# Kernel tuning notes

Measured on AMD Instinct MI355X. Metric: run time of the kernel, lower is better.

## Reference

```python
import jax, jax.numpy as jnp
import numpy as np

N, IN_DIM, HID, E = 2048, 128, 64, 32768
EPS = 1e-5  # torch BatchNorm1d / LayerNorm default eps


def setup_inputs() -> dict:
    key = jax.random.key(0)
    ks = jax.random.split(key, 12)
    s = 0.05
    return {
        "h": jax.random.normal(ks[0], (N, IN_DIM), jnp.float32),
        "local": jax.random.normal(ks[1], (N, IN_DIM), jnp.float32),
        "e": jax.random.normal(ks[2], (E, HID), jnp.float32),
        "src": jax.random.randint(ks[3], (E,), 0, N, jnp.int32),
        "dst": jax.random.randint(ks[4], (E,), 0, N, jnp.int32),
        "ln_w": jnp.ones((IN_DIM,), jnp.float32),
        "ln_b": jnp.zeros((IN_DIM,), jnp.float32),
        "conv_w": jax.random.normal(ks[5], (1, 2, 3), jnp.float32) * 0.3,
        "conv_b": jnp.zeros((1,), jnp.float32),
        "W1": jax.random.normal(ks[6], (IN_DIM, HID * HID), jnp.float32) * s,
        "b1": jnp.zeros((HID * HID,), jnp.float32),
        "Wp2": jax.random.normal(ks[7], (IN_DIM, HID), jnp.float32) * s,
        "bp2": jnp.zeros((HID,), jnp.float32),
        "W2": jax.random.normal(ks[8], (IN_DIM, HID), jnp.float32) * s,
        "b2": jnp.zeros((HID,), jnp.float32),
        "W3": jax.random.normal(ks[9], (HID, HID), jnp.float32) * s,
        "b3": jnp.zeros((HID,), jnp.float32),
        "bng_g": jnp.ones((HID,), jnp.float32),
        "bng_b": jnp.zeros((HID,), jnp.float32),
        "bnG_g": jnp.ones((HID,), jnp.float32),
        "bnG_b": jnp.zeros((HID,), jnp.float32),
        "bnL_g": jnp.ones((HID,), jnp.float32),
        "bnL_b": jnp.zeros((HID,), jnp.float32),
    }


def _bn_eval(x, g, b):
    # BatchNorm1d in eval mode, running_mean=0, running_var=1
    return x * (g / jnp.sqrt(1.0 + EPS)) + b


def _layernorm(x, w, b):
    mu = jnp.mean(x, axis=-1, keepdims=True)
    var = jnp.var(x, axis=-1, keepdims=True)
    return (x - mu) / jnp.sqrt(var + EPS) * w + b


def reference(h, local, e, src, dst, ln_w, ln_b, conv_w, conv_b,
              W1, b1, Wp2, bp2, W2, b2, W3, b3,
              bng_g, bng_b, bnG_g, bnG_b, bnL_g, bnL_b):
    # ---- local edge branch ----
    edge = jnp.stack([local[src], local[dst]], axis=1)  # [E, 2, in_dim]
    edge = _layernorm(edge, ln_w, ln_b)
    # Conv1d(2 -> 1, k=3, pad=1) over the in_dim axis
    lr_local = jax.lax.conv_general_dilated(
        edge, conv_w, window_strides=(1,), padding=[(1, 1)],
        dimension_numbers=("NCH", "OIH", "NCH"))[:, 0, :] + conv_b  # [E, in_dim]
    lr_local = jax.nn.relu(lr_local)  # dropout is identity in eval
    lr_local = lr_local @ W2 + b2  # [E, hid]

    # ---- global edge branch ----
    p1 = jax.nn.relu(h @ W1 + b1).reshape(h.shape[0], HID, HID)  # [N, hid(d), hid(k)]
    p2 = jax.nn.relu(h @ Wp2 + bp2)  # [N, hid(k)]
    # mm[i, j, d] = sum_k p1[i, d, k] * p2[j, k]; gather only needed edges
    lr_global = jnp.einsum("edk,ek->ed", p1[src], p2[dst])  # [E, hid]
    lr_global = _bn_eval(lr_global, bng_g, bng_b) @ W3 + b3
    lr_global = jax.nn.relu(_bn_eval(lr_global, bnG_g, bnG_b))

    lr_local = jax.nn.relu(_bn_eval(lr_local, bnL_g, bnL_b))
    return lr_local + lr_global + e
```

## Files before the change

kernel.cpp:

```cpp
#include <hip/hip_runtime.h>

#define N_NODES 2048
#define IN_DIM 128
#define HID 64
#define N_EDGES 32768
#define EPS 1e-5f

typedef short short8 __attribute__((ext_vector_type(8)));
typedef float f32x4 __attribute__((ext_vector_type(4)));

__device__ __forceinline__ float relu_f(float x) { return fmaxf(x, 0.f); }

__device__ __forceinline__ unsigned short f2bf(float f) {
  unsigned int u = __float_as_uint(f);
  u = (u + 0x7fffu + ((u >> 16) & 1u)) >> 16;
  return (unsigned short)u;
}
__device__ __forceinline__ float bf2f(unsigned short h) {
  return __uint_as_float(((unsigned int)h) << 16);
}
__device__ __forceinline__ short8 pack8(const float* f) {
  short8 o;
  #pragma unroll
  for (int i = 0; i < 8; ++i) o[i] = (short)f2bf(f[i]);
  return o;
}

__global__ __launch_bounds__(256) void ln_kernel(
    const float* __restrict__ local, const float* __restrict__ ln_w,
    const float* __restrict__ ln_b, float* __restrict__ out)
{
  int wave = threadIdx.x >> 6;
  int lane = threadIdx.x & 63;
  int row = blockIdx.x * 4 + wave;
  const float* x = local + (size_t)row * IN_DIM;
  float x0 = x[lane], x1 = x[lane + 64];
  float s1 = x0 + x1;
  float s2 = x0 * x0 + x1 * x1;
  #pragma unroll
  for (int off = 32; off > 0; off >>= 1) {
    s1 += __shfl_xor(s1, off);
    s2 += __shfl_xor(s2, off);
  }
  float mean = s1 * (1.f / IN_DIM);
  float var = s2 * (1.f / IN_DIM) - mean * mean;
  float rstd = rsqrtf(var + EPS);
  float* o = out + (size_t)row * IN_DIM;
  o[lane]      = (x0 - mean) * rstd * ln_w[lane] + ln_b[lane];
  o[lane + 64] = (x1 - mean) * rstd * ln_w[lane + 64] + ln_b[lane + 64];
}

__global__ __launch_bounds__(256) void p2_kernel(
    const float* __restrict__ h, const float* __restrict__ Wp2,
    const float* __restrict__ bp2, unsigned short* __restrict__ p2b)
{
  __shared__ float hs[4][IN_DIM];
  int wv = threadIdx.x >> 6, l = threadIdx.x & 63;
  int i = blockIdx.x * 4 + wv;
  hs[wv][l] = h[(size_t)i * IN_DIM + l];
  hs[wv][l + 64] = h[(size_t)i * IN_DIM + 64 + l];
  float acc = bp2[l];
  #pragma unroll 8
  for (int m = 0; m < IN_DIM; ++m) acc += hs[wv][m] * Wp2[m * HID + l];
  p2b[(size_t)i * HID + l] = f2bf(relu_f(acc));
}

__global__ __launch_bounds__(256) void prep_misc(
    const float* __restrict__ h, const float* __restrict__ W2,
    const float* __restrict__ W3, unsigned short* __restrict__ hb,
    unsigned short* __restrict__ w2tb, unsigned short* __restrict__ w3tb)
{
  int b = blockIdx.x, t = threadIdx.x;
  if (b < 256) {
    int idx = (b * 256 + t) * 4;
    float4 v = *(const float4*)(h + idx);
    ushort4 o;
    o.x = f2bf(v.x); o.y = f2bf(v.y); o.z = f2bf(v.z); o.w = f2bf(v.w);
    *(ushort4*)(hb + idx) = o;
  } else if (b == 256) {
    for (int i = t; i < IN_DIM * HID; i += 256) {
      int x = i >> 6, j = i & 63;
      w2tb[j * IN_DIM + x] = f2bf(W2[i]);
    }
  } else {
    for (int i = t; i < HID * HID; i += 256) {
      int k = i >> 6, j = i & 63;
      w3tb[j * HID + k] = f2bf(W3[i]);
    }
  }
}

__global__ __launch_bounds__(256) void tr_w1(
    const float* __restrict__ W1, unsigned short* __restrict__ w1t)
{
  __shared__ float tile[32][33];
  int n0 = blockIdx.x * 32, k0 = blockIdx.y * 32;
  int tx = threadIdx.x & 31, ty = threadIdx.x >> 5;
  #pragma unroll
  for (int r = 0; r < 4; ++r)
    tile[ty + 8 * r][tx] = W1[(size_t)(k0 + ty + 8 * r) * 4096 + n0 + tx];
  __syncthreads();
  #pragma unroll
  for (int r = 0; r < 4; ++r)
    w1t[(size_t)(n0 + ty + 8 * r) * 128 + k0 + tx] = f2bf(tile[tx][ty + 8 * r]);
}

__global__ __launch_bounds__(256) void p1_gemm(
    const unsigned short* __restrict__ hb,
    const unsigned short* __restrict__ w1t,
    const float* __restrict__ b1,
    unsigned short* __restrict__ p1b)
{
  int t = threadIdx.x;
  int w = t >> 6, l = t & 63;
  int lr = l & 15, lq = l >> 4;
  int bm = (blockIdx.x & 15) * 128;
  int bn = (blockIdx.x >> 4) * 128;
  int m0 = bm + w * 32;

  f32x4 acc[2][8];
  #pragma unroll
  for (int mi = 0; mi < 2; ++mi)
    #pragma unroll
    for (int ni = 0; ni < 8; ++ni) acc[mi][ni] = (f32x4){0.f, 0.f, 0.f, 0.f};

  #pragma unroll
  for (int k0 = 0; k0 < 128; k0 += 32) {
    short8 a[2], b[8];
    #pragma unroll
    for (int mi = 0; mi < 2; ++mi)
      a[mi] = *(const short8*)(hb + (size_t)(m0 + mi * 16 + lr) * 128 + k0 + lq * 8);
    #pragma unroll
    for (int ni = 0; ni < 8; ++ni)
      b[ni] = *(const short8*)(w1t + (size_t)(bn + ni * 16 + lr) * 128 + k0 + lq * 8);
    #pragma unroll
    for (int mi = 0; mi < 2; ++mi)
      #pragma unroll
      for (int ni = 0; ni < 8; ++ni)
        acc[mi][ni] = __builtin_amdgcn_mfma_f32_16x16x32_bf16(a[mi], b[ni], acc[mi][ni], 0, 0, 0);
  }

  #pragma unroll
  for (int mi = 0; mi < 2; ++mi)
    #pragma unroll
    for (int ni = 0; ni < 8; ++ni) {
      int col = bn + ni * 16 + lr;
      float bias = b1[col];
      #pragma unroll
      for (int r = 0; r < 4; ++r) {
        int row = m0 + mi * 16 + lq * 4 + r;
        p1b[(size_t)row * 4096 + col] = f2bf(relu_f(acc[mi][ni][r] + bias));
      }
    }
}

__global__ void hist_kernel(const int* __restrict__ src, int* __restrict__ cnt) {
  int e = blockIdx.x * 256 + threadIdx.x;
  atomicAdd(&cnt[src[e]], 1);
}

__global__ __launch_bounds__(256) void scan_kernel(
    const int* __restrict__ cnt, int* __restrict__ start,
    int* __restrict__ cursor, int* __restrict__ ptile)
{
  __shared__ int part[256];
  __shared__ int part2[256];
  int t = threadIdx.x;
  int loc[8], locT[8];
  int s = 0, s2 = 0;
  #pragma unroll
  for (int i = 0; i < 8; ++i) {
    int c = cnt[t * 8 + i];
    loc[i] = s;  s += c;
    locT[i] = s2; s2 += (c + 15) >> 4;
  }
  part[t] = s; part2[t] = s2;
  __syncthreads();
  for (int off = 1; off < 256; off <<= 1) {
    int v = (t >= off) ? part[t - off] : 0;
    int v2 = (t >= off) ? part2[t - off] : 0;
    __syncthreads();
    part[t] += v; part2[t] += v2;
    __syncthreads();
  }
  int base = (t == 0) ? 0 : part[t - 1];
  int base2 = (t == 0) ? 0 : part2[t - 1];
  #pragma unroll
  for (int i = 0; i < 8; ++i) {
    int v = base + loc[i];
    start[t * 8 + i] = v;
    cursor[t * 8 + i] = v;
    ptile[t * 8 + i] = base2 + locT[i];
  }
  if (t == 255) { start[N_NODES] = part[255]; ptile[N_NODES] = part2[255]; }
}

__global__ void scatter_kernel(const int* __restrict__ src,
                               int* __restrict__ cursor, int* __restrict__ perm) {
  int e = blockIdx.x * 256 + threadIdx.x;
  int p = atomicAdd(&cursor[src[e]], 1);
  perm[p] = e;
}

__global__ void build_tiles(const int* __restrict__ cnt, const int* __restrict__ start,
                            const int* __restrict__ ptile, const int* __restrict__ perm,
                            int* __restrict__ tile_src, int* __restrict__ perm_padded) {
  int i = blockIdx.x * 256 + threadIdx.x;
  int deg = cnt[i], s0 = start[i], t0 = ptile[i];
  int nt = (deg + 15) >> 4;
  for (int k = 0; k < nt; ++k) {
    int tid = t0 + k;
    tile_src[tid] = i;
    for (int j = 0; j < 16; ++j) {
      int pos = k * 16 + j;
      perm_padded[tid * 16 + j] = (pos < deg) ? perm[s0 + pos] : -1;
    }
  }
}

__global__ __launch_bounds__(256) void gather_mfma(
    const unsigned short* __restrict__ p1b, const unsigned short* __restrict__ p2b,
    const int* __restrict__ dst, const int* __restrict__ perm_padded,
    const int* __restrict__ tile_src, const int* __restrict__ ptile,
    const unsigned short* __restrict__ w3tb, const float* __restrict__ b3,
    const float* __restrict__ bng_g, const float* __restrict__ bng_b,
    const float* __restrict__ bnG_g, const float* __restrict__ bnG_b,
    float* __restrict__ gbuf)
{
  __shared__ float gs[4][16][68];
  const int t = threadIdx.x;
  const int w = t >> 6, l = t & 63;
  const int lr = l & 15, lq = l >> 4;
  const int n_tiles = ptile[N_NODES];
  const float rs = rsqrtf(1.f + EPS);

  float bngG[4], bngB[4], bnGG[4], bnGB[4], b3c[4];
  #pragma unroll
  for (int ni = 0; ni < 4; ++ni) {
    int col = ni * 16 + lr;
    bngG[ni] = bng_g[col] * rs; bngB[ni] = bng_b[col];
    bnGG[ni] = bnG_g[col] * rs; bnGB[ni] = bnG_b[col];
    b3c[ni] = b3[col];
  }

  for (int tile = blockIdx.x * 4 + w; tile < n_tiles; tile += gridDim.x * 4) {
    const int srcn = tile_src[tile];
    const int eidx = perm_padded[tile * 16 + lr];
    const int dn = (eidx >= 0) ? dst[eidx] : 0;

    const unsigned short* p2r = p2b + (size_t)dn * HID + lq * 8;
    short8 a0 = *(const short8*)(p2r);
    short8 a1 = *(const short8*)(p2r + 32);

    const unsigned short* pr = p1b + (size_t)srcn * 4096 + lr * 64 + lq * 8;
    f32x4 c[4];
    #pragma unroll
    for (int ni = 0; ni < 4; ++ni) {
      c[ni] = (f32x4){0.f, 0.f, 0.f, 0.f};
      short8 b0 = *(const short8*)(pr + ni * 1024);
      short8 b1 = *(const short8*)(pr + ni * 1024 + 32);
      c[ni] = __builtin_amdgcn_mfma_f32_16x16x32_bf16(a0, b0, c[ni], 0, 0, 0);
      c[ni] = __builtin_amdgcn_mfma_f32_16x16x32_bf16(a1, b1, c[ni], 0, 0, 0);
    }

    #pragma unroll
    for (int ni = 0; ni < 4; ++ni)
      #pragma unroll
      for (int r = 0; r < 4; ++r)
        gs[w][lq * 4 + r][ni * 16 + lr] = c[ni][r] * bngG[ni] + bngB[ni];
    asm volatile("s_waitcnt lgkmcnt(0)" ::: "memory");

    short8 ga0 = pack8(&gs[w][lr][lq * 8]);
    short8 ga1 = pack8(&gs[w][lr][32 + lq * 8]);

    const unsigned short* wr = w3tb + lr * HID + lq * 8;
    f32x4 u[4];
    #pragma unroll
    for (int ni = 0; ni < 4; ++ni) {
      u[ni] = (f32x4){0.f, 0.f, 0.f, 0.f};
      short8 b0 = *(const short8*)(wr + ni * 1024);
      short8 b1 = *(const short8*)(wr + ni * 1024 + 32);
      u[ni] = __builtin_amdgcn_mfma_f32_16x16x32_bf16(ga0, b0, u[ni], 0, 0, 0);
      u[ni] = __builtin_amdgcn_mfma_f32_16x16x32_bf16(ga1, b1, u[ni], 0, 0, 0);
    }

    int er[4];
    #pragma unroll
    for (int r = 0; r < 4; ++r) er[r] = perm_padded[tile * 16 + lq * 4 + r];
    #pragma unroll
    for (int ni = 0; ni < 4; ++ni) {
      int col = ni * 16 + lr;
      #pragma unroll
      for (int r = 0; r < 4; ++r)
        if (er[r] >= 0)
          gbuf[(size_t)er[r] * HID + col] =
              relu_f((u[ni][r] + b3c[ni]) * bnGG[ni] + bnGB[ni]);
    }
  }
}

__global__ __launch_bounds__(256) void final_kernel(
    const float* __restrict__ lnl, const int* __restrict__ src,
    const int* __restrict__ dst, const float* __restrict__ conv_w,
    const float* __restrict__ conv_b, const unsigned short* __restrict__ w2tb,
    const float* __restrict__ b2,
    const float* __restrict__ bnL_g, const float* __restrict__ bnL_b,
    const float* __restrict__ gbuf, const float* __restrict__ e_in,
    float* __restrict__ out)
{
  __shared__ float lns[32][132];
  __shared__ unsigned short rc[16][136];
  __shared__ int nodebuf[32];

  const int eb = blockIdx.x * 16;
  const int t = threadIdx.x;
  const int w = t >> 6, l = t & 63;
  const int lr = l & 15, lq = l >> 4;
  const float rs = rsqrtf(1.f + EPS);

  if (t < 32) nodebuf[t] = (t & 1) ? dst[eb + (t >> 1)] : src[eb + (t >> 1)];
  __syncthreads();
  #pragma unroll
  for (int r = 0; r < 4; ++r) {
    int flat = (r * 256 + t) * 4;
    int rr = flat >> 7, x = flat & 127;
    *(float4*)&lns[rr][x] = *(const float4*)(lnl + (size_t)nodebuf[rr] * IN_DIM + x);
  }
  __syncthreads();
  {
    float cw0 = conv_w[0], cw1 = conv_w[1], cw2 = conv_w[2];
    float cw3 = conv_w[3], cw4 = conv_w[4], cw5 = conv_w[5];
    float cb = conv_b[0];
    #pragma unroll
    for (int r = 0; r < 8; ++r) {
      int flat = r * 256 + t;
      int ei = flat >> 7, x = flat & 127;
      const float* a = &lns[2 * ei][0];
      const float* b = &lns[2 * ei + 1][0];
      float am = (x > 0) ? a[x - 1] : 0.f;
      float ap = (x < 127) ? a[x + 1] : 0.f;
      float bm = (x > 0) ? b[x - 1] : 0.f;
      float bp = (x < 127) ? b[x + 1] : 0.f;
      rc[ei][x] = f2bf(relu_f(cw0 * am + cw1 * a[x] + cw2 * ap +
                              cw3 * bm + cw4 * b[x] + cw5 * bp + cb));
    }
  }
  __syncthreads();
  f32x4 u = (f32x4){0.f, 0.f, 0.f, 0.f};
  #pragma unroll
  for (int ks = 0; ks < 4; ++ks) {
    short8 a = *(const short8*)&rc[lr][ks * 32 + lq * 8];
    short8 b = *(const short8*)(w2tb + (size_t)(w * 16 + lr) * IN_DIM + ks * 32 + lq * 8);
    u = __builtin_amdgcn_mfma_f32_16x16x32_bf16(a, b, u, 0, 0, 0);
  }
  int col = w * 16 + lr;
  float g = bnL_g[col] * rs, bb = bnL_b[col], b2c = b2[col];
  #pragma unroll
  for (int r = 0; r < 4; ++r) {
    int e = eb + lq * 4 + r;
    float vl = relu_f((u[r] + b2c) * g + bb);
    out[(size_t)e * HID + col] = vl + gbuf[(size_t)e * HID + col] + e_in[(size_t)e * HID + col];
  }
}

extern "C" void kernel_launch(void* const* d_in, const int* in_sizes, int n_in,
                              void* d_out, int out_size, void* d_ws, size_t ws_size,
                              hipStream_t stream) {
  const float* h      = (const float*)d_in[0];
  const float* local  = (const float*)d_in[1];
  const float* e_in   = (const float*)d_in[2];
  const int*   src    = (const int*)d_in[3];
  const int*   dst    = (const int*)d_in[4];
  const float* ln_w   = (const float*)d_in[5];
  const float* ln_b   = (const float*)d_in[6];
  const float* conv_w = (const float*)d_in[7];
  const float* conv_b = (const float*)d_in[8];
  const float* W1     = (const float*)d_in[9];
  const float* b1     = (const float*)d_in[10];
  const float* Wp2    = (const float*)d_in[11];
  const float* bp2    = (const float*)d_in[12];
  const float* W2     = (const float*)d_in[13];
  const float* b2     = (const float*)d_in[14];
  const float* W3     = (const float*)d_in[15];
  const float* b3     = (const float*)d_in[16];
  const float* bng_g  = (const float*)d_in[17];
  const float* bng_b  = (const float*)d_in[18];
  const float* bnG_g  = (const float*)d_in[19];
  const float* bnG_b  = (const float*)d_in[20];
  const float* bnL_g  = (const float*)d_in[21];
  const float* bnL_b  = (const float*)d_in[22];
  float* out = (float*)d_out;

  char* p = (char*)d_ws;
  unsigned short* p1b = (unsigned short*)p; p += (size_t)N_NODES * HID * HID * 2;
  unsigned short* p2b = (unsigned short*)p; p += (size_t)N_NODES * HID * 2;
  float* lnl  = (float*)p; p += (size_t)N_NODES * IN_DIM * 4;
  float* gbuf = (float*)p; p += (size_t)N_EDGES * HID * 4;
  unsigned short* hb   = (unsigned short*)p; p += (size_t)N_NODES * IN_DIM * 2;
  unsigned short* w1t  = (unsigned short*)p; p += (size_t)4096 * 128 * 2;
  unsigned short* w2tb = (unsigned short*)p; p += (size_t)HID * IN_DIM * 2;
  unsigned short* w3tb = (unsigned short*)p; p += (size_t)HID * HID * 2;
  int* cnt    = (int*)p; p += N_NODES * 4;
  int* cursor = (int*)p; p += N_NODES * 4;
  int* startb = (int*)p; p += (N_NODES + 1) * 4;
  int* ptile  = (int*)p; p += (N_NODES + 1) * 4;
  int* perm   = (int*)p; p += (size_t)N_EDGES * 4;
  int* tile_src    = (int*)p; p += 4096 * 4;
  int* perm_padded = (int*)p; p += (size_t)4096 * 16 * 4;

  hipMemsetAsync(cnt, 0, N_NODES * sizeof(int), stream);

  prep_misc<<<258, 256, 0, stream>>>(h, W2, W3, hb, w2tb, w3tb);
  tr_w1<<<dim3(128, 4), 256, 0, stream>>>(W1, w1t);
  ln_kernel<<<N_NODES / 4, 256, 0, stream>>>(local, ln_w, ln_b, lnl);
  p2_kernel<<<N_NODES / 4, 256, 0, stream>>>(h, Wp2, bp2, p2b);
  p1_gemm<<<512, 256, 0, stream>>>(hb, w1t, b1, p1b);
  hist_kernel<<<N_EDGES / 256, 256, 0, stream>>>(src, cnt);
  scan_kernel<<<1, 256, 0, stream>>>(cnt, startb, cursor, ptile);
  scatter_kernel<<<N_EDGES / 256, 256, 0, stream>>>(src, cursor, perm);
  build_tiles<<<N_NODES / 256, 256, 0, stream>>>(cnt, startb, ptile, perm, tile_src, perm_padded);
  gather_mfma<<<512, 256, 0, stream>>>(p1b, p2b, dst, perm_padded, tile_src, ptile,
                                       w3tb, b3, bng_g, bng_b, bnG_g, bnG_b, gbuf);
  final_kernel<<<N_EDGES / 16, 256, 0, stream>>>(lnl, src, dst, conv_w, conv_b,
                                                 w2tb, b2, bnL_g, bnL_b, gbuf, e_in, out);
}
```

Measured before the change: 188.0 us.

## Fuse local branch into edge MFMA kernel and merge prep kernels

Merges the separate prep kernels (bf16 casts, W1 transpose, layernorm, p2) into one launch. The local conv+W2 branch moves into the per-tile global edge kernel, so the fp32 gbuf round-trip and the final kernel disappear. Layernorm output is stored in bf16. The CSR build drops the perm/build_tiles pass and scatters straight into padded tiles. p1_gemm is retiled with swapped operands to allow vectorized bf16 stores. The cost is extra LDS traffic and a heavier edge kernel, plus a 0xFF memset of perm_padded.

```diff
diff --git a/kernel.cpp b/kernel.cpp
--- a/kernel.cpp
+++ b/kernel.cpp
@@ -5,6 +5,7 @@
 #define HID 64
 #define N_EDGES 32768
 #define EPS 1e-5f
+#define MAX_TILES 4608
 
 typedef short short8 __attribute__((ext_vector_type(8)));
 typedef float f32x4 __attribute__((ext_vector_type(4)));
@@ -26,83 +27,73 @@
   return o;
 }
 
-__global__ __launch_bounds__(256) void ln_kernel(
+__global__ __launch_bounds__(256) void prep_all(
+    const float* __restrict__ h, const float* __restrict__ W2,
+    const float* __restrict__ W3, const float* __restrict__ W1,
     const float* __restrict__ local, const float* __restrict__ ln_w,
-    const float* __restrict__ ln_b, float* __restrict__ out)
+    const float* __restrict__ ln_b, const float* __restrict__ Wp2,
+    const float* __restrict__ bp2,
+    unsigned short* __restrict__ hb, unsigned short* __restrict__ w2tb,
+    unsigned short* __restrict__ w3tb, unsigned short* __restrict__ w1t,
+    unsigned short* __restrict__ lnlb, unsigned short* __restrict__ p2b)
 {
-  int wave = threadIdx.x >> 6;
-  int lane = threadIdx.x & 63;
-  int row = blockIdx.x * 4 + wave;
-  const float* x = local + (size_t)row * IN_DIM;
-  float x0 = x[lane], x1 = x[lane + 64];
-  float s1 = x0 + x1;
-  float s2 = x0 * x0 + x1 * x1;
-  #pragma unroll
-  for (int off = 32; off > 0; off >>= 1) {
-    s1 += __shfl_xor(s1, off);
-    s2 += __shfl_xor(s2, off);
-  }
-  float mean = s1 * (1.f / IN_DIM);
-  float var = s2 * (1.f / IN_DIM) - mean * mean;
-  float rstd = rsqrtf(var + EPS);
-  float* o = out + (size_t)row * IN_DIM;
-  o[lane]      = (x0 - mean) * rstd * ln_w[lane] + ln_b[lane];
-  o[lane + 64] = (x1 - mean) * rstd * ln_w[lane + 64] + ln_b[lane + 64];
-}
-
-__global__ __launch_bounds__(256) void p2_kernel(
-    const float* __restrict__ h, const float* __restrict__ Wp2,
-    const float* __restrict__ bp2, unsigned short* __restrict__ p2b)
-{
+  __shared__ float tile[32][33];
   __shared__ float hs[4][IN_DIM];
-  int wv = threadIdx.x >> 6, l = threadIdx.x & 63;
-  int i = blockIdx.x * 4 + wv;
-  hs[wv][l] = h[(size_t)i * IN_DIM + l];
-  hs[wv][l + 64] = h[(size_t)i * IN_DIM + 64 + l];
-  float acc = bp2[l];
-  #pragma unroll 8
-  for (int m = 0; m < IN_DIM; ++m) acc += hs[wv][m] * Wp2[m * HID + l];
-  p2b[(size_t)i * HID + l] = f2bf(relu_f(acc));
-}
-
-__global__ __launch_bounds__(256) void prep_misc(
-    const float* __restrict__ h, const float* __restrict__ W2,
-    const float* __restrict__ W3, unsigned short* __restrict__ hb,
-    unsigned short* __restrict__ w2tb, unsigned short* __restrict__ w3tb)
-{
-  int b = blockIdx.x, t = threadIdx.x;
+  const int b = blockIdx.x, t = threadIdx.x;
+
   if (b < 256) {
     int idx = (b * 256 + t) * 4;
     float4 v = *(const float4*)(h + idx);
-    ushort4 o;
-    o.x = f2bf(v.x); o.y = f2bf(v.y); o.z = f2bf(v.z); o.w = f2bf(v.w);
+    ushort4 o; o.x = f2bf(v.x); o.y = f2bf(v.y); o.z = f2bf(v.z); o.w = f2bf(v.w);
     *(ushort4*)(hb + idx) = o;
   } else if (b == 256) {
     for (int i = t; i < IN_DIM * HID; i += 256) {
       int x = i >> 6, j = i & 63;
       w2tb[j * IN_DIM + x] = f2bf(W2[i]);
     }
-  } else {
+  } else if (b == 257) {
     for (int i = t; i < HID * HID; i += 256) {
       int k = i >> 6, j = i & 63;
       w3tb[j * HID + k] = f2bf(W3[i]);
     }
-  }
-}
-
-__global__ __launch_bounds__(256) void tr_w1(
-    const float* __restrict__ W1, unsigned short* __restrict__ w1t)
-{
-  __shared__ float tile[32][33];
-  int n0 = blockIdx.x * 32, k0 = blockIdx.y * 32;
-  int tx = threadIdx.x & 31, ty = threadIdx.x >> 5;
-  #pragma unroll
-  for (int r = 0; r < 4; ++r)
-    tile[ty + 8 * r][tx] = W1[(size_t)(k0 + ty + 8 * r) * 4096 + n0 + tx];
-  __syncthreads();
-  #pragma unroll
-  for (int r = 0; r < 4; ++r)
-    w1t[(size_t)(n0 + ty + 8 * r) * 128 + k0 + tx] = f2bf(tile[tx][ty + 8 * r]);
+  } else if (b < 258 + 512) {
+    int b2 = b - 258;
+    int n0 = (b2 & 127) * 32, k0 = (b2 >> 7) * 32;
+    int tx = t & 31, ty = t >> 5;
+    #pragma unroll
+    for (int r = 0; r < 4; ++r)
+      tile[ty + 8 * r][tx] = W1[(size_t)(k0 + ty + 8 * r) * 4096 + n0 + tx];
+    __syncthreads();
+    #pragma unroll
+    for (int r = 0; r < 4; ++r)
+      w1t[(size_t)(n0 + ty + 8 * r) * 128 + k0 + tx] = f2bf(tile[tx][ty + 8 * r]);
+  } else if (b < 770 + 512) {
+    int wave = t >> 6, lane = t & 63;
+    int row = (b - 770) * 4 + wave;
+    const float* x = local + (size_t)row * IN_DIM;
+    float x0 = x[lane], x1 = x[lane + 64];
+    float s1 = x0 + x1, s2 = x0 * x0 + x1 * x1;
+    #pragma unroll
+    for (int off = 32; off > 0; off >>= 1) {
+      s1 += __shfl_xor(s1, off);
+      s2 += __shfl_xor(s2, off);
+    }
+    float mean = s1 * (1.f / IN_DIM);
+    float var = s2 * (1.f / IN_DIM) - mean * mean;
+    float rstd = rsqrtf(var + EPS);
+    unsigned short* o = lnlb + (size_t)row * IN_DIM;
+    o[lane]      = f2bf((x0 - mean) * rstd * ln_w[lane] + ln_b[lane]);
+    o[lane + 64] = f2bf((x1 - mean) * rstd * ln_w[lane + 64] + ln_b[lane + 64]);
+  } else {
+    int wv = t >> 6, l = t & 63;
+    int i = (b - 1282) * 4 + wv;
+    hs[wv][l] = h[(size_t)i * IN_DIM + l];
+    hs[wv][l + 64] = h[(size_t)i * IN_DIM + 64 + l];
+    float acc = bp2[l];
+    #pragma unroll 8
+    for (int m = 0; m < IN_DIM; ++m) acc += hs[wv][m] * Wp2[m * HID + l];
+    p2b[(size_t)i * HID + l] = f2bf(relu_f(acc));
+  }
 }
 
 __global__ __launch_bounds__(256) void p1_gemm(
@@ -111,47 +102,38 @@
     const float* __restrict__ b1,
     unsigned short* __restrict__ p1b)
 {
-  int t = threadIdx.x;
-  int w = t >> 6, l = t & 63;
-  int lr = l & 15, lq = l >> 4;
-  int bm = (blockIdx.x & 15) * 128;
-  int bn = (blockIdx.x >> 4) * 128;
-  int m0 = bm + w * 32;
-
-  f32x4 acc[2][8];
-  #pragma unroll
-  for (int mi = 0; mi < 2; ++mi)
-    #pragma unroll
-    for (int ni = 0; ni < 8; ++ni) acc[mi][ni] = (f32x4){0.f, 0.f, 0.f, 0.f};
+  const int t = threadIdx.x;
+  const int w = t >> 6, l = t & 63;
+  const int lr = l & 15, lq = l >> 4;
+  const int bm = (blockIdx.x & 31) * 64;
+  const int bn = (blockIdx.x >> 5) * 128;
+  const int m0 = bm + w * 16;
+
+  f32x4 acc[8];
+  #pragma unroll
+  for (int ni = 0; ni < 8; ++ni) acc[ni] = (f32x4){0.f, 0.f, 0.f, 0.f};
 
   #pragma unroll
   for (int k0 = 0; k0 < 128; k0 += 32) {
-    short8 a[2], b[8];
-    #pragma unroll
-    for (int mi = 0; mi < 2; ++mi)
-      a[mi] = *(const short8*)(hb + (size_t)(m0 + mi * 16 + lr) * 128 + k0 + lq * 8);
-    #pragma unroll
-    for (int ni = 0; ni < 8; ++ni)
-      b[ni] = *(const short8*)(w1t + (size_t)(bn + ni * 16 + lr) * 128 + k0 + lq * 8);
-    #pragma unroll
-    for (int mi = 0; mi < 2; ++mi)
-      #pragma unroll
-      for (int ni = 0; ni < 8; ++ni)
-        acc[mi][ni] = __builtin_amdgcn_mfma_f32_16x16x32_bf16(a[mi], b[ni], acc[mi][ni], 0, 0, 0);
-  }
-
-  #pragma unroll
-  for (int mi = 0; mi < 2; ++mi)
+    short8 bmf = *(const short8*)(hb + (size_t)(m0 + lr) * 128 + k0 + lq * 8);
     #pragma unroll
     for (int ni = 0; ni < 8; ++ni) {
-      int col = bn + ni * 16 + lr;
-      float bias = b1[col];
-      #pragma unroll
-      for (int r = 0; r < 4; ++r) {
-        int row = m0 + mi * 16 + lq * 4 + r;
-        p1b[(size_t)row * 4096 + col] = f2bf(relu_f(acc[mi][ni][r] + bias));
-      }
-    }
+      short8 a = *(const short8*)(w1t + (size_t)(bn + ni * 16 + lr) * 128 + k0 + lq * 8);
+      acc[ni] = __builtin_amdgcn_mfma_f32_16x16x32_bf16(a, bmf, acc[ni], 0, 0, 0);
+    }
+  }
+  const int m = m0 + lr;
+  #pragma unroll
+  for (int ni = 0; ni < 8; ++ni) {
+    int n = bn + ni * 16 + lq * 4;
+    float4 bv = *(const float4*)&b1[n];
+    ushort4 o;
+    o.x = f2bf(relu_f(acc[ni][0] + bv.x));
+    o.y = f2bf(relu_f(acc[ni][1] + bv.y));
+    o.z = f2bf(relu_f(acc[ni][2] + bv.z));
+    o.w = f2bf(relu_f(acc[ni][3] + bv.w));
+    *(ushort4*)&p1b[(size_t)m * 4096 + n] = o;
+  }
 }
 
 __global__ void hist_kernel(const int* __restrict__ src, int* __restrict__ cnt) {
@@ -160,107 +142,107 @@
 }
 
 __global__ __launch_bounds__(256) void scan_kernel(
-    const int* __restrict__ cnt, int* __restrict__ start,
-    int* __restrict__ cursor, int* __restrict__ ptile)
+    const int* __restrict__ cnt, int* __restrict__ ptile, int* __restrict__ tile_src)
 {
-  __shared__ int part[256];
   __shared__ int part2[256];
   int t = threadIdx.x;
-  int loc[8], locT[8];
-  int s = 0, s2 = 0;
+  int locT[8];
+  int s2 = 0;
   #pragma unroll
   for (int i = 0; i < 8; ++i) {
-    int c = cnt[t * 8 + i];
-    loc[i] = s;  s += c;
-    locT[i] = s2; s2 += (c + 15) >> 4;
-  }
-  part[t] = s; part2[t] = s2;
+    locT[i] = s2;
+    s2 += (cnt[t * 8 + i] + 15) >> 4;
+  }
+  part2[t] = s2;
   __syncthreads();
   for (int off = 1; off < 256; off <<= 1) {
-    int v = (t >= off) ? part[t - off] : 0;
-    int v2 = (t >= off) ? part2[t - off] : 0;
+    int v = (t >= off) ? part2[t - off] : 0;
     __syncthreads();
-    part[t] += v; part2[t] += v2;
+    part2[t] += v;
     __syncthreads();
   }
-  int base = (t == 0) ? 0 : part[t - 1];
   int base2 = (t == 0) ? 0 : part2[t - 1];
   #pragma unroll
   for (int i = 0; i < 8; ++i) {
-    int v = base + loc[i];
-    start[t * 8 + i] = v;
-    cursor[t * 8 + i] = v;
-    ptile[t * 8 + i] = base2 + locT[i];
-  }
-  if (t == 255) { start[N_NODES] = part[255]; ptile[N_NODES] = part2[255]; }
-}
-
-__global__ void scatter_kernel(const int* __restrict__ src,
-                               int* __restrict__ cursor, int* __restrict__ perm) {
+    int node = t * 8 + i;
+    int tb = base2 + locT[i];
+    ptile[node] = tb;
+    int nt = (cnt[node] + 15) >> 4;
+    for (int k = 0; k < nt; ++k) tile_src[tb + k] = node;
+  }
+  if (t == 255) ptile[N_NODES] = part2[255];
+}
+
+__global__ void scatter_kernel(const int* __restrict__ src, const int* __restrict__ ptile,
+                               int* __restrict__ cursor, int* __restrict__ perm_padded) {
   int e = blockIdx.x * 256 + threadIdx.x;
-  int p = atomicAdd(&cursor[src[e]], 1);
-  perm[p] = e;
-}
-
-__global__ void build_tiles(const int* __restrict__ cnt, const int* __restrict__ start,
-                            const int* __restrict__ ptile, const int* __restrict__ perm,
-                            int* __restrict__ tile_src, int* __restrict__ perm_padded) {
-  int i = blockIdx.x * 256 + threadIdx.x;
-  int deg = cnt[i], s0 = start[i], t0 = ptile[i];
-  int nt = (deg + 15) >> 4;
-  for (int k = 0; k < nt; ++k) {
-    int tid = t0 + k;
-    tile_src[tid] = i;
-    for (int j = 0; j < 16; ++j) {
-      int pos = k * 16 + j;
-      perm_padded[tid * 16 + j] = (pos < deg) ? perm[s0 + pos] : -1;
-    }
-  }
-}
-
-__global__ __launch_bounds__(256) void gather_mfma(
+  int s = src[e];
+  int r = atomicAdd(&cursor[s], 1);
+  perm_padded[ptile[s] * 16 + r] = e;
+}
+
+__global__ __launch_bounds__(256) void edge_mfma(
     const unsigned short* __restrict__ p1b, const unsigned short* __restrict__ p2b,
+    const unsigned short* __restrict__ lnlb,
     const int* __restrict__ dst, const int* __restrict__ perm_padded,
     const int* __restrict__ tile_src, const int* __restrict__ ptile,
-    const unsigned short* __restrict__ w3tb, const float* __restrict__ b3,
+    const unsigned short* __restrict__ w2tb, const unsigned short* __restrict__ w3tb,
+    const float* __restrict__ conv_w, const float* __restrict__ conv_b,
+    const float* __restrict__ b2, const float* __restrict__ b3,
     const float* __restrict__ bng_g, const float* __restrict__ bng_b,
     const float* __restrict__ bnG_g, const float* __restrict__ bnG_b,
-    float* __restrict__ gbuf)
+    const float* __restrict__ bnL_g, const float* __restrict__ bnL_b,
+    const float* __restrict__ e_in, float* __restrict__ out)
 {
   __shared__ float gs[4][16][68];
+  __shared__ unsigned short ln1s[4][16][136];
+  __shared__ unsigned short ln0s[4][136];
+
   const int t = threadIdx.x;
   const int w = t >> 6, l = t & 63;
   const int lr = l & 15, lq = l >> 4;
   const int n_tiles = ptile[N_NODES];
   const float rs = rsqrtf(1.f + EPS);
 
-  float bngG[4], bngB[4], bnGG[4], bnGB[4], b3c[4];
+  float bngG[4], bngB[4], bnGG[4], bnGB[4], b3c[4], bnLG[4], bnLB[4], b2c[4];
   #pragma unroll
   for (int ni = 0; ni < 4; ++ni) {
     int col = ni * 16 + lr;
     bngG[ni] = bng_g[col] * rs; bngB[ni] = bng_b[col];
     bnGG[ni] = bnG_g[col] * rs; bnGB[ni] = bnG_b[col];
-    b3c[ni] = b3[col];
-  }
+    bnLG[ni] = bnL_g[col] * rs; bnLB[ni] = bnL_b[col];
+    b3c[ni] = b3[col]; b2c[ni] = b2[col];
+  }
+  const float cw0 = conv_w[0], cw1 = conv_w[1], cw2 = conv_w[2];
+  const float cw3 = conv_w[3], cw4 = conv_w[4], cw5 = conv_w[5];
+  const float cb = conv_b[0];
 
   for (int tile = blockIdx.x * 4 + w; tile < n_tiles; tile += gridDim.x * 4) {
     const int srcn = tile_src[tile];
     const int eidx = perm_padded[tile * 16 + lr];
     const int dn = (eidx >= 0) ? dst[eidx] : 0;
 
+    {
+      const unsigned short* r1 = lnlb + (size_t)dn * IN_DIM + lq * 32;
+      #pragma unroll
+      for (int c2 = 0; c2 < 4; ++c2)
+        *(uint4*)&ln1s[w][lr][lq * 32 + c2 * 8] = *(const uint4*)(r1 + c2 * 8);
+      if (l < 32)
+        *(ushort4*)&ln0s[w][l * 4] = *(const ushort4*)(lnlb + (size_t)srcn * IN_DIM + l * 4);
+    }
+
     const unsigned short* p2r = p2b + (size_t)dn * HID + lq * 8;
     short8 a0 = *(const short8*)(p2r);
     short8 a1 = *(const short8*)(p2r + 32);
-
     const unsigned short* pr = p1b + (size_t)srcn * 4096 + lr * 64 + lq * 8;
     f32x4 c[4];
     #pragma unroll
     for (int ni = 0; ni < 4; ++ni) {
       c[ni] = (f32x4){0.f, 0.f, 0.f, 0.f};
-      short8 b0 = *(const short8*)(pr + ni * 1024);
-      short8 b1 = *(const short8*)(pr + ni * 1024 + 32);
-      c[ni] = __builtin_amdgcn_mfma_f32_16x16x32_bf16(a0, b0, c[ni], 0, 0, 0);
-      c[ni] = __builtin_amdgcn_mfma_f32_16x16x32_bf16(a1, b1, c[ni], 0, 0, 0);
+      short8 pb0 = *(const short8*)(pr + ni * 1024);
+      short8 pb1 = *(const short8*)(pr + ni * 1024 + 32);
+      c[ni] = __builtin_amdgcn_mfma_f32_16x16x32_bf16(a0, pb0, c[ni], 0, 0, 0);
+      c[ni] = __builtin_amdgcn_mfma_f32_16x16x32_bf16(a1, pb1, c[ni], 0, 0, 0);
     }
 
     #pragma unroll
@@ -269,97 +251,63 @@
       for (int r = 0; r < 4; ++r)
         gs[w][lq * 4 + r][ni * 16 + lr] = c[ni][r] * bngG[ni] + bngB[ni];
     asm volatile("s_waitcnt lgkmcnt(0)" ::: "memory");
-
     short8 ga0 = pack8(&gs[w][lr][lq * 8]);
     short8 ga1 = pack8(&gs[w][lr][32 + lq * 8]);
 
-    const unsigned short* wr = w3tb + lr * HID + lq * 8;
+    const unsigned short* wr3 = w3tb + lr * HID + lq * 8;
     f32x4 u[4];
     #pragma unroll
     for (int ni = 0; ni < 4; ++ni) {
       u[ni] = (f32x4){0.f, 0.f, 0.f, 0.f};
-      short8 b0 = *(const short8*)(wr + ni * 1024);
-      short8 b1 = *(const short8*)(wr + ni * 1024 + 32);
-      u[ni] = __builtin_amdgcn_mfma_f32_16x16x32_bf16(ga0, b0, u[ni], 0, 0, 0);
-      u[ni] = __builtin_amdgcn_mfma_f32_16x16x32_bf16(ga1, b1, u[ni], 0, 0, 0);
+      short8 wb0 = *(const short8*)(wr3 + ni * 1024);
+      short8 wb1 = *(const short8*)(wr3 + ni * 1024 + 32);
+      u[ni] = __builtin_amdgcn_mfma_f32_16x16x32_bf16(ga0, wb0, u[ni], 0, 0, 0);
+      u[ni] = __builtin_amdgcn_mfma_f32_16x16x32_bf16(ga1, wb1, u[ni], 0, 0, 0);
+    }
+
+    asm volatile("s_waitcnt vmcnt(0) lgkmcnt(0)" ::: "memory");
+    f32x4 v[4];
+    #pragma unroll
+    for (int ni = 0; ni < 4; ++ni) v[ni] = (f32x4){0.f, 0.f, 0.f, 0.f};
+    #pragma unroll
+    for (int ks = 0; ks < 4; ++ks) {
+      short8 af;
+      #pragma unroll
+      for (int j = 0; j < 8; ++j) {
+        int x = ks * 32 + lq * 8 + j;
+        float am = (x > 0)   ? bf2f(ln0s[w][x - 1]) : 0.f;
+        float az = bf2f(ln0s[w][x]);
+        float ap = (x < 127) ? bf2f(ln0s[w][x + 1]) : 0.f;
+        float bm = (x > 0)   ? bf2f(ln1s[w][lr][x - 1]) : 0.f;
+        float bz = bf2f(ln1s[w][lr][x]);
+        float bp = (x < 127) ? bf2f(ln1s[w][lr][x + 1]) : 0.f;
+        float cv = relu_f(cw0 * am + cw1 * az + cw2 * ap +
+                          cw3 * bm + cw4 * bz + cw5 * bp + cb);
+        af[j] = (short)f2bf(cv);
+      }
+      #pragma unroll
+      for (int ni = 0; ni < 4; ++ni) {
+        short8 wb = *(const short8*)(w2tb + (size_t)(ni * 16 + lr) * IN_DIM + ks * 32 + lq * 8);
+        v[ni] = __builtin_amdgcn_mfma_f32_16x16x32_bf16(af, wb, v[ni], 0, 0, 0);
+      }
     }
 
     int er[4];
     #pragma unroll
-    for (int r = 0; r < 4; ++r) er[r] = perm_padded[tile * 16 + lq * 4 + r];
+    for (int r = 0; r < 4; ++r) er[r] = __shfl(eidx, lq * 4 + r);
     #pragma unroll
     for (int ni = 0; ni < 4; ++ni) {
       int col = ni * 16 + lr;
       #pragma unroll
-      for (int r = 0; r < 4; ++r)
-        if (er[r] >= 0)
-          gbuf[(size_t)er[r] * HID + col] =
-              relu_f((u[ni][r] + b3c[ni]) * bnGG[ni] + bnGB[ni]);
-    }
-  }
-}
-
-__global__ __launch_bounds__(256) void final_kernel(
-    const float* __restrict__ lnl, const int* __restrict__ src,
-    const int* __restrict__ dst, const float* __restrict__ conv_w,
-    const float* __restrict__ conv_b, const unsigned short* __restrict__ w2tb,
-    const float* __restrict__ b2,
-    const float* __restrict__ bnL_g, const float* __restrict__ bnL_b,
-    const float* __restrict__ gbuf, const float* __restrict__ e_in,
-    float* __restrict__ out)
-{
-  __shared__ float lns[32][132];
-  __shared__ unsigned short rc[16][136];
-  __shared__ int nodebuf[32];
-
-  const int eb = blockIdx.x * 16;
-  const int t = threadIdx.x;
-  const int w = t >> 6, l = t & 63;
-  const int lr = l & 15, lq = l >> 4;
-  const float rs = rsqrtf(1.f + EPS);
-
-  if (t < 32) nodebuf[t] = (t & 1) ? dst[eb + (t >> 1)] : src[eb + (t >> 1)];
-  __syncthreads();
-  #pragma unroll
-  for (int r = 0; r < 4; ++r) {
-    int flat = (r * 256 + t) * 4;
-    int rr = flat >> 7, x = flat & 127;
-    *(float4*)&lns[rr][x] = *(const float4*)(lnl + (size_t)nodebuf[rr] * IN_DIM + x);
-  }
-  __syncthreads();
-  {
-    float cw0 = conv_w[0], cw1 = conv_w[1], cw2 = conv_w[2];
-    float cw3 = conv_w[3], cw4 = conv_w[4], cw5 = conv_w[5];
-    float cb = conv_b[0];
-    #pragma unroll
-    for (int r = 0; r < 8; ++r) {
-      int flat = r * 256 + t;
-      int ei = flat >> 7, x = flat & 127;
-      const float* a = &lns[2 * ei][0];
-      const float* b = &lns[2 * ei + 1][0];
-      float am = (x > 0) ? a[x - 1] : 0.f;
-      float ap = (x < 127) ? a[x + 1] : 0.f;
-      float bm = (x > 0) ? b[x - 1] : 0.f;
-      float bp = (x < 127) ? b[x + 1] : 0.f;
-      rc[ei][x] = f2bf(relu_f(cw0 * am + cw1 * a[x] + cw2 * ap +
-                              cw3 * bm + cw4 * b[x] + cw5 * bp + cb));
-    }
-  }
-  __syncthreads();
-  f32x4 u = (f32x4){0.f, 0.f, 0.f, 0.f};
-  #pragma unroll
-  for (int ks = 0; ks < 4; ++ks) {
-    short8 a = *(const short8*)&rc[lr][ks * 32 + lq * 8];
-    short8 b = *(const short8*)(w2tb + (size_t)(w * 16 + lr) * IN_DIM + ks * 32 + lq * 8);
-    u = __builtin_amdgcn_mfma_f32_16x16x32_bf16(a, b, u, 0, 0, 0);
-  }
-  int col = w * 16 + lr;
-  float g = bnL_g[col] * rs, bb = bnL_b[col], b2c = b2[col];
-  #pragma unroll
-  for (int r = 0; r < 4; ++r) {
-    int e = eb + lq * 4 + r;
-    float vl = relu_f((u[r] + b2c) * g + bb);
-    out[(size_t)e * HID + col] = vl + gbuf[(size_t)e * HID + col] + e_in[(size_t)e * HID + col];
+      for (int r = 0; r < 4; ++r) {
+        int e = er[r];
+        if (e >= 0) {
+          float vg = relu_f((u[ni][r] + b3c[ni]) * bnGG[ni] + bnGB[ni]);
+          float vl = relu_f((v[ni][r] + b2c[ni]) * bnLG[ni] + bnLB[ni]);
+          out[(size_t)e * HID + col] = vl + vg + e_in[(size_t)e * HID + col];
+        }
+      }
+    }
   }
 }
 
@@ -392,35 +340,29 @@
   float* out = (float*)d_out;
 
   char* p = (char*)d_ws;
-  unsigned short* p1b = (unsigned short*)p; p += (size_t)N_NODES * HID * HID * 2;
-  unsigned short* p2b = (unsigned short*)p; p += (size_t)N_NODES * HID * 2;
-  float* lnl  = (float*)p; p += (size_t)N_NODES * IN_DIM * 4;
-  float* gbuf = (float*)p; p += (size_t)N_EDGES * HID * 4;
+  unsigned short* p1b  = (unsigned short*)p; p += (size_t)N_NODES * HID * HID * 2;
+  unsigned short* p2b  = (unsigned short*)p; p += (size_t)N_NODES * HID * 2;
+  unsigned short* lnlb = (unsigned short*)p; p += (size_t)N_NODES * IN_DIM * 2;
   unsigned short* hb   = (unsigned short*)p; p += (size_t)N_NODES * IN_DIM * 2;
   unsigned short* w1t  = (unsigned short*)p; p += (size_t)4096 * 128 * 2;
   unsigned short* w2tb = (unsigned short*)p; p += (size_t)HID * IN_DIM * 2;
   unsigned short* w3tb = (unsigned short*)p; p += (size_t)HID * HID * 2;
   int* cnt    = (int*)p; p += N_NODES * 4;
   int* cursor = (int*)p; p += N_NODES * 4;
-  int* startb = (int*)p; p += (N_NODES + 1) * 4;
   int* ptile  = (int*)p; p += (N_NODES + 1) * 4;
-  int* perm   = (int*)p; p += (size_t)N_EDGES * 4;
-  int* tile_src    = (int*)p; p += 4096 * 4;
-  int* perm_padded = (int*)p; p += (size_t)4096 * 16 * 4;
-
-  hipMemsetAsync(cnt, 0, N_NODES * sizeof(int), stream);
-
-  prep_misc<<<258, 256, 0, stream>>>(h, W2, W3, hb, w2tb, w3tb);
-  tr_w1<<<dim3(128, 4), 256, 0, stream>>>(W1, w1t);
-  ln_kernel<<<N_NODES / 4, 256, 0, stream>>>(local, ln_w, ln_b, lnl);
-  p2_kernel<<<N_NODES / 4, 256, 0, stream>>>(h, Wp2, bp2, p2b);
-  p1_gemm<<<512, 256, 0, stream>>>(hb, w1t, b1, p1b);
+  int* tile_src    = (int*)p; p += MAX_TILES * 4;
+  int* perm_padded = (int*)p; p += (size_t)MAX_TILES * 16 * 4;
+
+  hipMemsetAsync(cnt, 0, 2 * N_NODES * sizeof(int), stream);
+  hipMemsetAsync(perm_padded, 0xFF, (size_t)MAX_TILES * 16 * sizeof(int), stream);
+
+  prep_all<<<1794, 256, 0, stream>>>(h, W2, W3, W1, local, ln_w, ln_b, Wp2, bp2,
+                                     hb, w2tb, w3tb, w1t, lnlb, p2b);
   hist_kernel<<<N_EDGES / 256, 256, 0, stream>>>(src, cnt);
-  scan_kernel<<<1, 256, 0, stream>>>(cnt, startb, cursor, ptile);
-  scatter_kernel<<<N_EDGES / 256, 256, 0, stream>>>(src, cursor, perm);
-  build_tiles<<<N_NODES / 256, 256, 0, stream>>>(cnt, startb, ptile, perm, tile_src, perm_padded);
-  gather_mfma<<<512, 256, 0, stream>>>(p1b, p2b, dst, perm_padded, tile_src, ptile,
-                                       w3tb, b3, bng_g, bng_b, bnG_g, bnG_b, gbuf);
-  final_kernel<<<N_EDGES / 16, 256, 0, stream>>>(lnl, src, dst, conv_w, conv_b,
-                                                 w2tb, b2, bnL_g, bnL_b, gbuf, e_in, out);
-}
+  p1_gemm<<<1024, 256, 0, stream>>>(hb, w1t, b1, p1b);
+  scan_kernel<<<1, 256, 0, stream>>>(cnt, ptile, tile_src);
+  scatter_kernel<<<N_EDGES / 256, 256, 0, stream>>>(src, ptile, cursor, perm_padded);
+  edge_mfma<<<768, 256, 0, stream>>>(p1b, p2b, lnlb, dst, perm_padded, tile_src, ptile,
+                                     w2tb, w3tb, conv_w, conv_b, b2, b3,
+                                     bng_g, bng_b, bnG_g, bnG_b, bnL_g, bnL_b, e_in, out);
+}
```

Result: slower. 192.9 us (+2.6%).
